# Kernel optimization log

Measured on AMD Instinct MI355X. Metric: run time of the kernel, lower is better.

## Reference

```python
import jax, jax.numpy as jnp
import numpy as np

WIRES = 4
N_LAYERS = 2
NUM_CLASSES = 10


def _apply_ry(state, c, s, axis):
    # state: [N,2,2,2,2]; apply Ry with cos/sin halves c,s on given qubit axis.
    st = jnp.moveaxis(state, axis, -1)
    a0, a1 = st[..., 0], st[..., 1]
    st = jnp.stack([c * a0 - s * a1, s * a0 + c * a1], axis=-1)
    return jnp.moveaxis(st, -1, axis)


def _cnot(state, ctrl, tgt):
    st = jnp.moveaxis(state, (ctrl, tgt), (-2, -1))
    st = jnp.stack([st[..., 0, :], st[..., 1, ::-1]], axis=-2)
    return jnp.moveaxis(st, (-2, -1), (ctrl, tgt))


def _simulate(angles, params):
    # angles: [N,4] encoding Ry angles; params: [L,4]. Returns PauliZ expvals [N,4].
    N = angles.shape[0]
    state = jnp.zeros((N, 2, 2, 2, 2), dtype=angles.dtype).at[:, 0, 0, 0, 0].set(1.0)
    half = angles * 0.5
    for i in range(WIRES):
        c = jnp.cos(half[:, i])[:, None, None, None]
        s = jnp.sin(half[:, i])[:, None, None, None]
        state = _apply_ry(state, c, s, 1 + i)
    for l in range(params.shape[0]):
        for i in range(WIRES):
            th = params[l, i] * 0.5
            state = _apply_ry(state, jnp.cos(th), jnp.sin(th), 1 + i)
        for i in range(WIRES - 1):
            state = _cnot(state, 1 + i, 2 + i)
        state = _cnot(state, WIRES, 1)  # CNOT(last, 0)
    probs = state ** 2
    sign = jnp.array([1.0, -1.0], dtype=angles.dtype)
    zs = [jnp.einsum('nabcd,' + 'abcd'[i] + '->n', probs, sign) for i in range(WIRES)]
    return jnp.stack(zs, axis=1)


def setup_inputs() -> dict:
    key = jax.random.key(0)
    k1, k2, k3, k4 = jax.random.split(key, 4)
    B = 8192
    x = jax.random.uniform(k1, (B, 28, 28), dtype=jnp.float32)
    params = jax.random.normal(k2, (N_LAYERS, WIRES), dtype=jnp.float32)
    W = jax.random.normal(k3, (NUM_CLASSES, WIRES * 14 * 14), dtype=jnp.float32) * 0.02
    b = jnp.zeros((NUM_CLASSES,), dtype=jnp.float32)
    return {"x": x, "params": params, "W": W, "b": b}


def reference(x, params, W, b):
    B = x.shape[0]
    # Extract 2x2 patches in row-major order: [B,196,4] matching torch loop.
    angles = x.reshape(B, 14, 2, 14, 2).transpose(0, 1, 3, 2, 4).reshape(B * 196, 4)
    feats = _simulate(angles, params).reshape(B, 196 * WIRES)  # [B,784]
    logits = feats @ W.T + b
    return jax.nn.log_softmax(logits, axis=-1)
```

## Files before the change

kernel.cpp:

```cpp
#include <hip/hip_runtime.h>


template <int BIT>
static __device__ __forceinline__ void apply_ry_tan(float (&a)[16], float t) {
#pragma unroll
    for (int i = 0; i < 16; ++i) {
        if (i & (1 << BIT)) continue;
        float a0 = a[i];
        float a1 = a[i | (1 << BIT)];
        a[i]              = fmaf(-t, a1, a0);
        a[i | (1 << BIT)] = fmaf( t, a0, a1);
    }
}

template <int CBIT, int TBIT>
static __device__ __forceinline__ void apply_cnot(float (&a)[16]) {
#pragma unroll
    for (int i = 0; i < 16; ++i) {
        if ((i & (1 << CBIT)) && !(i & (1 << TBIT))) {
            float t = a[i];
            a[i] = a[i | (1 << TBIT)];
            a[i | (1 << TBIT)] = t;
        }
    }
}

__global__ __launch_bounds__(512, 4) void quanv_fused_kernel(
    const float* __restrict__ x,
    const float* __restrict__ params,
    const float* __restrict__ W,
    const float* __restrict__ bias,
    float* __restrict__ out,
    int B)
{
    __shared__ float Wl[10 * 784];

    {
        const float4* Wg4 = (const float4*)W;
        float4* Wl4 = (float4*)Wl;
        for (int t = threadIdx.x; t < 1960; t += 512) Wl4[t] = Wg4[t];
    }
    __syncthreads();

    const int lane = threadIdx.x & 63;
    const int lid  = lane & 31;
    const int wave = threadIdx.x >> 6;
    const int row  = blockIdx.x * 16 + wave * 2 + (lane >> 5);
    if (row >= B) return;

    float h0[4], t1w[4];
    float scale2 = 1.0f;
#pragma unroll
    for (int w = 0; w < 4; ++w) {
        h0[w] = 0.5f * params[w];
        float s, c;
        __sincosf(0.5f * params[4 + w], &s, &c);
        t1w[w] = s / c;
        scale2 *= c;
    }
    scale2 *= scale2;

    float logit[10];
#pragma unroll
    for (int c = 0; c < 10; ++c) logit[c] = 0.0f;

    const float* xrow = x + (size_t)row * 784;

    int i = lid / 14;
    int j = lid - i * 14;
    int ai = i * 56 + j * 2;
    float2 c0 = *(const float2*)(xrow + ai);
    float2 c1 = *(const float2*)(xrow + ai + 28);

#pragma unroll 1
    for (int p = lid; p < 196; p += 32) {
        j += 4; i += 2;
        if (j >= 14) { j -= 14; ++i; }
        const int an = (i < 14) ? (i * 56 + j * 2) : ai;
        const float2 n0 = *(const float2*)(xrow + an);
        const float2 n1 = *(const float2*)(xrow + an + 28);

        float e0, s0, e1, s1, e2, s2, e3, s3;
        __sincosf(fmaf(0.5f, c0.x, h0[0]), &s0, &e0);
        __sincosf(fmaf(0.5f, c0.y, h0[1]), &s1, &e1);
        __sincosf(fmaf(0.5f, c1.x, h0[2]), &s2, &e2);
        __sincosf(fmaf(0.5f, c1.y, h0[3]), &s3, &e3);

        float p01[4] = {e0 * e1, e0 * s1, s0 * e1, s0 * s1};
        float p23[4] = {e2 * e3, e2 * s3, s2 * e3, s2 * s3};
        float amp[16];
#pragma unroll
        for (int idx = 0; idx < 16; ++idx)
            amp[idx] = p01[idx >> 2] * p23[idx & 3];

        apply_cnot<3, 2>(amp);
        apply_cnot<2, 1>(amp);
        apply_cnot<1, 0>(amp);
        apply_cnot<0, 3>(amp);
        apply_ry_tan<3>(amp, t1w[0]);
        apply_ry_tan<2>(amp, t1w[1]);
        apply_ry_tan<1>(amp, t1w[2]);
        apply_ry_tan<0>(amp, t1w[3]);
        apply_cnot<3, 2>(amp);
        apply_cnot<2, 1>(amp);
        apply_cnot<1, 0>(amp);
        apply_cnot<0, 3>(amp);

        float pr[16];
#pragma unroll
        for (int idx = 0; idx < 16; ++idx) pr[idx] = amp[idx] * amp[idx];

        float sp[8], dp[8];
#pragma unroll
        for (int k = 0; k < 8; ++k) {
            sp[k] = pr[2 * k] + pr[2 * k + 1];
            dp[k] = pr[2 * k] - pr[2 * k + 1];
        }
        float z3 = ((dp[0] + dp[1]) + (dp[2] + dp[3])) + ((dp[4] + dp[5]) + (dp[6] + dp[7]));
        float t[4], u[4];
#pragma unroll
        for (int k = 0; k < 4; ++k) {
            t[k] = sp[2 * k] + sp[2 * k + 1];
            u[k] = sp[2 * k] - sp[2 * k + 1];
        }
        float z2 = (u[0] + u[1]) + (u[2] + u[3]);
        float z1 = (t[0] - t[1]) + (t[2] - t[3]);
        float z0 = (t[0] + t[1]) - (t[2] + t[3]);

        const float* wp = Wl + 4 * p;
#pragma unroll
        for (int c = 0; c < 10; ++c) {
            float4 wv = *(const float4*)(wp + c * 784);
            logit[c] = fmaf(z0, wv.x, fmaf(z1, wv.y, fmaf(z2, wv.z, fmaf(z3, wv.w, logit[c]))));
        }

        c0 = n0; c1 = n1; ai = an;
    }

#pragma unroll
    for (int off = 16; off > 0; off >>= 1) {
#pragma unroll
        for (int c = 0; c < 10; ++c)
            logit[c] += __shfl_xor(logit[c], off, 64);
    }

    if (lid == 0) {
        float v[10];
        float m = -1e30f;
#pragma unroll
        for (int c = 0; c < 10; ++c) {
            v[c] = fmaf(scale2, logit[c], bias[c]);
            m = fmaxf(m, v[c]);
        }
        float sum = 0.f;
#pragma unroll
        for (int c = 0; c < 10; ++c) sum += __expf(v[c] - m);
        float lse = m + __logf(sum);

        float2* o = (float2*)(out + (size_t)row * 10);
#pragma unroll
        for (int k = 0; k < 5; ++k)
            o[k] = make_float2(v[2 * k] - lse, v[2 * k + 1] - lse);
    }
}

extern "C" void kernel_launch(void* const* d_in, const int* in_sizes, int n_in,
                              void* d_out, int out_size, void* d_ws, size_t ws_size,
                              hipStream_t stream) {
    const float* x      = (const float*)d_in[0];
    const float* params = (const float*)d_in[1];
    const float* W      = (const float*)d_in[2];
    const float* bias   = (const float*)d_in[3];
    float* out          = (float*)d_out;

    const int B = in_sizes[0] / 784;
    const int blocks = (B + 15) / 16;

    hipLaunchKernelGGL(quanv_fused_kernel, dim3(blocks), dim3(512), 0, stream,
                       x, params, W, bias, out, B);
}
```

Measured before the change: 84.77 us.

## Replace statevector simulation with closed-form PauliZ expectation polynomials

```diff
diff --git a/kernel.cpp b/kernel.cpp
--- a/kernel.cpp
+++ b/kernel.cpp
@@ -1,29 +1,5 @@
 #include <hip/hip_runtime.h>
 
-
-template <int BIT>
-static __device__ __forceinline__ void apply_ry_tan(float (&a)[16], float t) {
-#pragma unroll
-    for (int i = 0; i < 16; ++i) {
-        if (i & (1 << BIT)) continue;
-        float a0 = a[i];
-        float a1 = a[i | (1 << BIT)];
-        a[i]              = fmaf(-t, a1, a0);
-        a[i | (1 << BIT)] = fmaf( t, a0, a1);
-    }
-}
-
-template <int CBIT, int TBIT>
-static __device__ __forceinline__ void apply_cnot(float (&a)[16]) {
-#pragma unroll
-    for (int i = 0; i < 16; ++i) {
-        if ((i & (1 << CBIT)) && !(i & (1 << TBIT))) {
-            float t = a[i];
-            a[i] = a[i | (1 << TBIT)];
-            a[i | (1 << TBIT)] = t;
-        }
-    }
-}
 
 __global__ __launch_bounds__(512, 4) void quanv_fused_kernel(
     const float* __restrict__ x,
@@ -48,17 +24,29 @@
     const int row  = blockIdx.x * 16 + wave * 2 + (lane >> 5);
     if (row >= B) return;
 
-    float h0[4], t1w[4];
-    float scale2 = 1.0f;
+    const float t0w0 = params[0], t0w1 = params[1], t0w2 = params[2], t0w3 = params[3];
+    float cB[4], sB[4];
 #pragma unroll
-    for (int w = 0; w < 4; ++w) {
-        h0[w] = 0.5f * params[w];
-        float s, c;
-        __sincosf(0.5f * params[4 + w], &s, &c);
-        t1w[w] = s / c;
-        scale2 *= c;
-    }
-    scale2 *= scale2;
+    for (int w = 0; w < 4; ++w) __sincosf(params[4 + w], &sB[3 - w], &cB[3 - w]);
+
+    const float k0a =  cB[0] * cB[1] * cB[2];
+    const float k0b = -cB[0] * cB[1] * sB[2];
+    const float k0c = -sB[0] * cB[1] * cB[2];
+    const float k0d = -sB[0] * sB[1] * sB[2];
+    const float k1a =  cB[2] * cB[3];
+    const float k1b =  sB[2] * sB[3];
+    const float k2a =  cB[1] * cB[2] * cB[3];
+    const float k2b = -cB[1] * cB[2] * sB[3];
+    const float k2c = -cB[1] * sB[2] * cB[3];
+    const float k2d = -sB[1] * sB[2] * sB[3];
+    const float k3a =  cB[0] * cB[1] * cB[2] * cB[3];
+    const float k3b =  cB[0] * cB[1] * sB[2] * sB[3];
+    const float k3c = -cB[0] * sB[1] * cB[2] * cB[3];
+    const float k3d =  cB[0] * sB[1] * sB[2] * cB[3];
+    const float k3e =  sB[0] * cB[1] * cB[2] * sB[3];
+    const float k3f = -sB[0] * sB[1] * cB[2] * sB[3];
+    const float k3g = -sB[0] * sB[1] * sB[2] * cB[3];
+    const float k3h =  sB[0] * sB[1] * sB[2] * sB[3];
 
     float logit[10];
 #pragma unroll
@@ -69,8 +57,8 @@
     int i = lid / 14;
     int j = lid - i * 14;
     int ai = i * 56 + j * 2;
-    float2 c0 = *(const float2*)(xrow + ai);
-    float2 c1 = *(const float2*)(xrow + ai + 28);
+    float2 v0 = *(const float2*)(xrow + ai);
+    float2 v1 = *(const float2*)(xrow + ai + 28);
 
 #pragma unroll 1
     for (int p = lid; p < 196; p += 32) {
@@ -80,52 +68,42 @@
         const float2 n0 = *(const float2*)(xrow + an);
         const float2 n1 = *(const float2*)(xrow + an + 28);
 
-        float e0, s0, e1, s1, e2, s2, e3, s3;
-        __sincosf(fmaf(0.5f, c0.x, h0[0]), &s0, &e0);
-        __sincosf(fmaf(0.5f, c0.y, h0[1]), &s1, &e1);
-        __sincosf(fmaf(0.5f, c1.x, h0[2]), &s2, &e2);
-        __sincosf(fmaf(0.5f, c1.y, h0[3]), &s3, &e3);
+        float C0, S0, C1, S1, C2, S2, C3, S3;
+        __sincosf(v0.x + t0w0, &S3, &C3);
+        __sincosf(v0.y + t0w1, &S2, &C2);
+        __sincosf(v1.x + t0w2, &S1, &C1);
+        __sincosf(v1.y + t0w3, &S0, &C0);
 
-        float p01[4] = {e0 * e1, e0 * s1, s0 * e1, s0 * s1};
-        float p23[4] = {e2 * e3, e2 * s3, s2 * e3, s2 * s3};
-        float amp[16];
-#pragma unroll
-        for (int idx = 0; idx < 16; ++idx)
-            amp[idx] = p01[idx >> 2] * p23[idx & 3];
+        const float C0C2 = C0 * C2, C0C1 = C0 * C1, C1C3 = C1 * C3, C2C3 = C2 * C3;
+        const float S1S2 = S1 * S2, S2S3 = S2 * S3, S1S3 = S1 * S3;
+        const float S0S1 = S0 * S1, S0S2 = S0 * S2, S0S3 = S0 * S3;
+        const float S0C1 = S0 * C1;
+        const float C0C2C3   = C0C2 * C3;
+        const float C0S1S2   = C0 * S1S2;
+        const float C0S1S2C3 = C0S1S2 * C3;
+        const float S0C1S2S3 = S0C1 * S2S3;
+        const float C0C1C3   = C0C1 * C3;
+        const float C1S2S3   = C1 * S2S3;
+        const float C0S1S3   = C0 * S1S3;
+        const float S0S1C2   = S0S1 * C2;
+        const float S0S2C3   = S0S2 * C3;
+        const float S1C2C3   = S1 * C2C3;
+        const float C0C1C2S3 = (C0C1 * C2) * S3;
 
-        apply_cnot<3, 2>(amp);
-        apply_cnot<2, 1>(amp);
-        apply_cnot<1, 0>(amp);
-        apply_cnot<0, 3>(amp);
-        apply_ry_tan<3>(amp, t1w[0]);
-        apply_ry_tan<2>(amp, t1w[1]);
-        apply_ry_tan<1>(amp, t1w[2]);
-        apply_ry_tan<0>(amp, t1w[3]);
-        apply_cnot<3, 2>(amp);
-        apply_cnot<2, 1>(amp);
-        apply_cnot<1, 0>(amp);
-        apply_cnot<0, 3>(amp);
-
-        float pr[16];
-#pragma unroll
-        for (int idx = 0; idx < 16; ++idx) pr[idx] = amp[idx] * amp[idx];
-
-        float sp[8], dp[8];
-#pragma unroll
-        for (int k = 0; k < 8; ++k) {
-            sp[k] = pr[2 * k] + pr[2 * k + 1];
-            dp[k] = pr[2 * k] - pr[2 * k + 1];
-        }
-        float z3 = ((dp[0] + dp[1]) + (dp[2] + dp[3])) + ((dp[4] + dp[5]) + (dp[6] + dp[7]));
-        float t[4], u[4];
-#pragma unroll
-        for (int k = 0; k < 4; ++k) {
-            t[k] = sp[2 * k] + sp[2 * k + 1];
-            u[k] = sp[2 * k] - sp[2 * k + 1];
-        }
-        float z2 = (u[0] + u[1]) + (u[2] + u[3]);
-        float z1 = (t[0] - t[1]) + (t[2] - t[3]);
-        float z0 = (t[0] + t[1]) - (t[2] + t[3]);
+        const float z0 = fmaf(k0a, C0C2C3,
+                         fmaf(k0b, C0S1S2,
+                         fmaf(k0c, S0C1S2S3, k0d * S3)));
+        const float z1 = fmaf(k1a, C0C1C3, k1b * S1S3);
+        const float z2 = fmaf(k2a, C0C2,
+                         fmaf(k2b, C1S2S3,
+                         fmaf(k2c, C0S1S2C3, k2d * S0S3)));
+        const float z3 = fmaf(k3a, C1C3,
+                         fmaf(k3b, C0S1S3,
+                         fmaf(k3c, S0S1C2,
+                         fmaf(k3d, S0S2C3,
+                         fmaf(k3e, S0C1,
+                         fmaf(k3f, S1C2C3,
+                         fmaf(k3g, C0C1C2S3, k3h * S2)))))));
 
         const float* wp = Wl + 4 * p;
 #pragma unroll
@@ -134,7 +112,7 @@
             logit[c] = fmaf(z0, wv.x, fmaf(z1, wv.y, fmaf(z2, wv.z, fmaf(z3, wv.w, logit[c]))));
         }
 
-        c0 = n0; c1 = n1; ai = an;
+        v0 = n0; v1 = n1; ai = an;
     }
 
 #pragma unroll
@@ -149,7 +127,7 @@
         float m = -1e30f;
 #pragma unroll
         for (int c = 0; c < 10; ++c) {
-            v[c] = fmaf(scale2, logit[c], bias[c]);
+            v[c] = logit[c] + bias[c];
             m = fmaxf(m, v[c]);
         }
         float sum = 0.f;
```

Measured after the change: 79.36 us. -6.4%, faster.
